# Kernel optimization log

Measured on AMD Instinct MI355X. Metric: run time of the kernel, lower is better.

Reference implementation:

```python
import jax, jax.numpy as jnp
import numpy as np
import math

B, T, D, H, V, L = 8, 512, 128, 512, 50257, 8
DT = 1.0
RAW_INIT = math.log(math.expm1(1.0))  # so softplus(raw) == 1.0


def setup_inputs() -> dict:
    key = jax.random.key(0)
    ks = jax.random.split(key, 8)
    x = jax.random.randint(ks[0], (B, T), 0, V)
    E = jax.random.normal(ks[1], (V, D), jnp.float32) * 0.02
    P = jax.random.normal(ks[2], (T, D), jnp.float32) * 0.01
    W0 = jax.random.normal(ks[3], (2 * D, H), jnp.float32) * 0.02
    W1 = jax.random.normal(ks[4], (H, H), jnp.float32) * 0.02
    W2 = jax.random.normal(ks[5], (H, H), jnp.float32) * 0.02
    W3 = jax.random.normal(ks[6], (H, 1), jnp.float32) * 0.002
    return {
        'x': x, 'E': E, 'P': P,
        'W0': W0, 'b0': jnp.zeros((H,), jnp.float32),
        'W1': W1, 'b1': jnp.zeros((H,), jnp.float32),
        'W2': W2, 'b2': jnp.zeros((H,), jnp.float32),
        'W3': W3, 'b3': jnp.zeros((1,), jnp.float32),
        'raw_m_bias': jnp.asarray(RAW_INIT, jnp.float32),
        'raw_gamma': jnp.asarray(RAW_INIT, jnp.float32),
    }


def causal_cumulative_mean(h):
    t = h.shape[1]
    denom = jnp.arange(1, t + 1, dtype=h.dtype)[None, :, None]
    return jnp.cumsum(h, axis=1) / denom


def mlp_energy_sum(xi, h, W0, b0, W1, b1, W2, b2, W3, b3):
    z = jnp.concatenate([xi, h], axis=-1)  # (B,T,2D)
    z = jax.nn.gelu(z @ W0 + b0, approximate=False)
    z = jax.nn.gelu(z @ W1 + b1, approximate=False)
    z = jax.nn.gelu(z @ W2 + b2, approximate=False)
    return jnp.sum(z @ W3 + b3)


def reference(x, E, P, W0, b0, W1, b1, W2, b2, W3, b3, raw_m_bias, raw_gamma):
    emb = E[x] + P[None, :T]  # (B,T,D)
    gamma = jax.nn.softplus(raw_gamma)
    m = jax.nn.softplus(raw_m_bias) + 0.001  # global mass
    h = emb
    v = jnp.zeros_like(h)
    for _ in range(L):
        # causal_force=True: xi built from detached h
        xi = causal_cumulative_mean(jax.lax.stop_gradient(h))
        grad_V = jax.grad(
            lambda hh: mlp_energy_sum(xi, hh, W0, b0, W1, b1, W2, b2, W3, b3)
        )(h)
        f = -grad_V
        v = (v + DT * f / m) / (1.0 + DT * gamma)
        h = h + DT * v
    logits = jnp.einsum('btd,vd->btv', h, E)  # (B,T,V)
    return logits
```

## Files before the change

### kernel.cpp

```cpp
#include <hip/hip_runtime.h>
#include <hip/hip_bf16.h>

typedef __attribute__((ext_vector_type(8))) short short8;
typedef __attribute__((ext_vector_type(4))) float f32x4;

#define DEV static __device__ __forceinline__

DEV void gelu_pair(float x, float& z, float& dz){
  float ax = fabsf(x)*0.70710678118654752f;
  float e  = __expf(-ax*ax);
  float t  = __fdividef(1.0f, 1.0f + 0.3275911f*ax);
  float poly = t*(0.254829592f + t*(-0.284496736f + t*(1.421413741f +
               t*(-1.453152027f + t*1.061405429f))));
  float erfv = 1.0f - poly*e;
  erfv = x < 0.0f ? -erfv : erfv;
  float cdf = 0.5f*(1.0f + erfv);
  z  = x*cdf;
  dz = cdf + x*0.39894228040143268f*e;
}
DEV float dgelu_f(float x){ float zz, dz; gelu_pair(x, zz, dz); return dz; }
DEV float softplus_f(float x){ return log1pf(expf(x)); }
DEV void store_f4_a4(float* p, f32x4 v){ __builtin_memcpy(p, &v, 16); }

DEV void gload_lds16(const __hip_bfloat16* g, __hip_bfloat16* l){
  __builtin_amdgcn_global_load_lds((const __attribute__((address_space(1))) void*)g,
                                   (__attribute__((address_space(3))) void*)l, 16, 0, 0);
}

DEV unsigned pack2bf(float a, float b){
  __hip_bfloat16 ba = __float2bfloat16(a), bb = __float2bfloat16(b);
  unsigned short ua, ub;
  __builtin_memcpy(&ua, &ba, 2); __builtin_memcpy(&ub, &bb, 2);
  return (unsigned)ua | ((unsigned)ub << 16);
}
DEV float unp_lo(unsigned u){ union{unsigned x; float f;} c; c.x = u << 16; return c.f; }
DEV float unp_hi(unsigned u){ union{unsigned x; float f;} c; c.x = u & 0xffff0000u; return c.f; }

__global__ __launch_bounds__(512) void embed_k(const int* __restrict__ x,
                        const float* __restrict__ E, const float* __restrict__ P,
                        float* __restrict__ h, float* __restrict__ S){
  int bid = blockIdx.x;
  int row = threadIdx.x >> 5;
  int q   = threadIdx.x & 31;
  int tok = bid*16 + row;
  int t   = tok & 511;
  int id  = x[tok];
  float4 e4 = ((const float4*)E)[(size_t)id*32 + q];
  float4 p4 = ((const float4*)P)[(size_t)t*32 + q];
  float4 val; val.x=e4.x+p4.x; val.y=e4.y+p4.y; val.z=e4.z+p4.z; val.w=e4.w+p4.w;
  ((float4*)h)[(size_t)tok*32 + q] = val;
  __shared__ float4 ps[16][32];
  ps[row][q] = val;
  __syncthreads();
  if (row==0){
    float4 s = ps[0][q];
    #pragma unroll
    for (int r=1;r<16;r++){
      float4 t4 = ps[r][q];
      s.x+=t4.x; s.y+=t4.y; s.z+=t4.z; s.w+=t4.w;
    }
    ((float4*)S)[(size_t)bid*32 + q] = s;
  }
}

__global__ void convw_k(const float* __restrict__ W0, const float* __restrict__ W1,
                        const float* __restrict__ W2,
                        __hip_bfloat16* __restrict__ W0T, __hip_bfloat16* __restrict__ W1T,
                        __hip_bfloat16* __restrict__ W2T, __hip_bfloat16* __restrict__ W2b,
                        __hip_bfloat16* __restrict__ W1b, __hip_bfloat16* __restrict__ W0h){
  int i = blockIdx.x*256 + threadIdx.x;
  if (i < 131072){
    int e=i&7, n=(i>>3)&511, kk=i>>12; int k=(kk>>2)*32+(kk&3)*8+e;
    W0T[i]=__float2bfloat16(W0[(size_t)k*512+n]);
  } else if (i < 393216){
    int j=i-131072; int e=j&7, n=(j>>3)&511, kk=j>>12; int k=(kk>>2)*32+(kk&3)*8+e;
    W1T[j]=__float2bfloat16(W1[(size_t)k*512+n]);
  } else if (i < 655360){
    int j=i-393216; int e=j&7, n=(j>>3)&511, kk=j>>12; int k=(kk>>2)*32+(kk&3)*8+e;
    W2T[j]=__float2bfloat16(W2[(size_t)k*512+n]);
  } else if (i < 917504){
    int j=i-655360; int e=j&7, n=(j>>3)&511, kk=j>>12; int k=(kk>>2)*32+(kk&3)*8+e;
    W2b[j]=__float2bfloat16(W2[(size_t)n*512+k]);
  } else if (i < 1179648){
    int j=i-917504; int e=j&7, n=(j>>3)&511, kk=j>>12; int k=(kk>>2)*32+(kk&3)*8+e;
    W1b[j]=__float2bfloat16(W1[(size_t)n*512+k]);
  } else if (i < 1245184){
    int j=i-1179648; int e=j&7, n=(j>>3)&127, kk=j>>10; int k=(kk>>2)*32+(kk&3)*8+e;
    W0h[j]=__float2bfloat16(W0[(size_t)(128+n)*512+k]);
  }
}
__global__ void conv_c4_k(const float* __restrict__ W, __hip_bfloat16* __restrict__ Wb, int n4){
  int i = blockIdx.x*256 + threadIdx.x;
  if (i < n4){
    float4 f = ((const float4*)W)[i];
    Wb[4*i+0]=__float2bfloat16(f.x);
    Wb[4*i+1]=__float2bfloat16(f.y);
    Wb[4*i+2]=__float2bfloat16(f.z);
    Wb[4*i+3]=__float2bfloat16(f.w);
  }
}

struct LayerP {
  const __hip_bfloat16 *W0T,*W1T,*W2T,*W2b,*W1b,*W0h;
  const float *b0,*b1,*b2,*W3;
  float *v, *h; __hip_bfloat16* hbf;
  const float* Sprev; float* Snext;
  const float *rawm,*rawg;
  int first, last;
};

template<int KSTEPS, int NW, int NF>
DEV void wpre(const __hip_bfloat16* __restrict__ Wt, int nbase, int r16, int g, int rot,
              short8 (&bb)[6][NF]){
  const __hip_bfloat16* wp = Wt + ((size_t)g*NW + nbase + r16)*8;
  #pragma unroll
  for (int d=0; d<5; d++){
    if (d < KSTEPS){
      int dd = (d + rot) & (KSTEPS-1);
      #pragma unroll
      for (int f=0; f<NF; f++)
        bb[d][f] = *(const short8*)&wp[((size_t)dd*4*NW + (size_t)f*16)*8];
    }
  }
}

template<int KSTEPS, int NW, int NF>
DEV void gphase(const __hip_bfloat16* __restrict__ Wt,
                const __hip_bfloat16* __restrict__ zin,
                int nbase, int r16, int g, int rot, f32x4 (&acc)[NF],
                short8 (&bb)[6][NF]){
  #pragma unroll
  for (int f=0;f<NF;f++) acc[f] = (f32x4){0.f,0.f,0.f,0.f};
  const __hip_bfloat16* wp = Wt + ((size_t)g*NW + nbase + r16)*8;
  #pragma unroll
  for (int s=0; s<KSTEPS; s++){
    if (s+5 < KSTEPS){
      int ss5 = (s + 5 + rot) & (KSTEPS-1);
      const __hip_bfloat16* wn = wp + (size_t)ss5*4*NW*8;
      #pragma unroll
      for (int f=0; f<NF; f++)
        bb[(s+5)%6][f] = *(const short8*)&wn[(size_t)f*128];
    }
    int ss = (s + rot) & (KSTEPS-1);
    short8 a = *(const short8*)&zin[(ss*4+g)*128 + r16*8];
    #pragma unroll
    for (int f=0; f<NF; f++)
      acc[f] = __builtin_amdgcn_mfma_f32_16x16x32_bf16(a, bb[s%6][f], acc[f],0,0,0);
  }
}

__global__ __launch_bounds__(1024,4) void layer_k(LayerP p){
  __shared__ __align__(16) __hip_bfloat16 sZ[2][8192];
  __shared__ float4 psum[16][32];
  __shared__ float4 psumC[16][32];
  const int tid = threadIdx.x;
  const int w = tid >> 6, lane = tid & 63;
  const int r16 = lane & 15, g = lane >> 4;
  const int rb = blockIdx.x;
  const int nb = w*32;
  const int rot = (rb >> 3) & 15;

  short8 bb[6][2];

  wpre<8,512,2>(p.W0T, nb, r16, g, rot, bb);
  float vr[4] = {0.f,0.f,0.f,0.f}, hr[4] = {0.f,0.f,0.f,0.f};
  float im = 0.f, fac = 0.f;
  if (w < 8){
    const int col = w*16 + r16;
    #pragma unroll
    for (int j=0;j<4;j++){
      size_t o = ((size_t)rb*16 + g*4 + j)*128 + col;
      hr[j] = p.h[o];
      vr[j] = p.first ? 0.f : p.v[o];
    }
    im  = 1.0f/(softplus_f(p.rawm[0]) + 0.001f);
    fac = 1.0f/(1.0f + softplus_f(p.rawg[0]));
  }

  if (tid < 512){
    const int row = tid >> 5;
    const int lane32 = tid & 31;
    const int b = rb >> 5, c = rb & 31;
    const float4* S4 = (const float4*)(p.Sprev + (size_t)b*32*128) + lane32;
    float4 part = {0.f,0.f,0.f,0.f};
    if (row < c){
      float4 t = S4[(size_t)row*32];
      part.x+=t.x; part.y+=t.y; part.z+=t.z; part.w+=t.w;
    }
    if (row+16 < c){
      float4 t = S4[(size_t)(row+16)*32];
      part.x+=t.x; part.y+=t.y; part.z+=t.z; part.w+=t.w;
    }
    float4 myrow = ((const float4*)(p.h + (size_t)rb*16*128))[(size_t)row*32 + lane32];
    psum[row][lane32]  = myrow;
    psumC[row][lane32] = part;
    __syncthreads();
    float4 pfx = {0.f,0.f,0.f,0.f};
    #pragma unroll
    for (int r=0;r<16;r++){
      float4 t = psumC[r][lane32];
      pfx.x+=t.x; pfx.y+=t.y; pfx.z+=t.z; pfx.w+=t.w;
    }
    #pragma unroll
    for (int rr=0; rr<15; rr++){
      float4 t = psum[rr][lane32];
      float sel = rr < row ? 1.0f : 0.0f;
      pfx.x += sel*t.x; pfx.y += sel*t.y; pfx.z += sel*t.z; pfx.w += sel*t.w;
    }
    pfx.x+=myrow.x; pfx.y+=myrow.y; pfx.z+=myrow.z; pfx.w+=myrow.w;
    float inv = 1.0f/(float)(c*16 + row + 1);
    const int d0 = lane32*4;
    union { ushort4 v; __hip_bfloat16 e[4]; } ux, uh;
    ux.e[0]=__float2bfloat16(pfx.x*inv); ux.e[1]=__float2bfloat16(pfx.y*inv);
    ux.e[2]=__float2bfloat16(pfx.z*inv); ux.e[3]=__float2bfloat16(pfx.w*inv);
    uh.e[0]=__float2bfloat16(myrow.x); uh.e[1]=__float2bfloat16(myrow.y);
    uh.e[2]=__float2bfloat16(myrow.z); uh.e[3]=__float2bfloat16(myrow.w);
    *(ushort4*)&sZ[0][(d0>>3)*128      + row*8 + (d0&7)] = ux.v;
    *(ushort4*)&sZ[0][(16+(d0>>3))*128 + row*8 + (d0&7)] = uh.v;
  } else {
    __syncthreads();
  }
  __syncthreads();

  f32x4 acc[2];
  unsigned g1p[2][2], g2p[2][2];

  gphase<8,512,2>(p.W0T, sZ[0], nb, r16, g, rot, acc, bb);
  wpre<16,512,2>(p.W1T, nb, r16, g, rot, bb);
  #pragma unroll
  for (int f=0; f<2; f++){
    int n = nb + f*16 + r16;
    float bias = p.b0[n];
    #pragma unroll
    for (int jp=0; jp<2; jp++){
      float z0, dz0, z1v, dz1;
      gelu_pair(acc[f][2*jp]   + bias, z0,  dz0);
      gelu_pair(acc[f][2*jp+1] + bias, z1v, dz1);
      g1p[f][jp] = pack2bf(dz0, dz1);
      sZ[1][(n>>3)*128 + (g*4+2*jp)*8   + (n&7)] = __float2bfloat16(z0);
      sZ[1][(n>>3)*128 + (g*4+2*jp+1)*8 + (n&7)] = __float2bfloat16(z1v);
    }
  }
  __syncthreads();

  gphase<16,512,2>(p.W1T, sZ[1], nb, r16, g, rot, acc, bb);
  wpre<16,512,2>(p.W2T, nb, r16, g, rot, bb);
  #pragma unroll
  for (int f=0; f<2; f++){
    int n = nb + f*16 + r16;
    float bias = p.b1[n];
    #pragma unroll
    for (int jp=0; jp<2; jp++){
      float z0, dz0, z1v, dz1;
      gelu_pair(acc[f][2*jp]   + bias, z0,  dz0);
      gelu_pair(acc[f][2*jp+1] + bias, z1v, dz1);
      g2p[f][jp] = pack2bf(dz0, dz1);
      sZ[0][(n>>3)*128 + (g*4+2*jp)*8   + (n&7)] = __float2bfloat16(z0);
      sZ[0][(n>>3)*128 + (g*4+2*jp+1)*8 + (n&7)] = __float2bfloat16(z1v);
    }
  }
  __syncthreads();

  gphase<16,512,2>(p.W2T, sZ[0], nb, r16, g, rot, acc, bb);
  wpre<16,512,2>(p.W2b, nb, r16, g, rot, bb);
  #pragma unroll
  for (int f=0; f<2; f++){
    int n = nb + f*16 + r16;
    float bias = p.b2[n];
    float w3 = p.W3[n];
    #pragma unroll
    for (int j=0;j<4;j++){
      float xx = acc[f][j] + bias;
      sZ[1][(n>>3)*128 + (g*4+j)*8 + (n&7)] = __float2bfloat16(w3*dgelu_f(xx));
    }
  }
  __syncthreads();

  gphase<16,512,2>(p.W2b, sZ[1], nb, r16, g, rot, acc, bb);
  wpre<16,512,2>(p.W1b, nb, r16, g, rot, bb);
  #pragma unroll
  for (int f=0; f<2; f++){
    int n = nb + f*16 + r16;
    #pragma unroll
    for (int jp=0; jp<2; jp++){
      float gv0 = unp_lo(g2p[f][jp]), gv1 = unp_hi(g2p[f][jp]);
      sZ[0][(n>>3)*128 + (g*4+2*jp)*8   + (n&7)] = __float2bfloat16(acc[f][2*jp]*gv0);
      sZ[0][(n>>3)*128 + (g*4+2*jp+1)*8 + (n&7)] = __float2bfloat16(acc[f][2*jp+1]*gv1);
    }
  }
  __syncthreads();

  gphase<16,512,2>(p.W1b, sZ[0], nb, r16, g, rot, acc, bb);
  short8 bbF[6][1];
  if (w < 8) wpre<16,128,1>(p.W0h, w*16, r16, g, rot, bbF);
  #pragma unroll
  for (int f=0; f<2; f++){
    int n = nb + f*16 + r16;
    #pragma unroll
    for (int jp=0; jp<2; jp++){
      float gv0 = unp_lo(g1p[f][jp]), gv1 = unp_hi(g1p[f][jp]);
      sZ[1][(n>>3)*128 + (g*4+2*jp)*8   + (n&7)] = __float2bfloat16(acc[f][2*jp]*gv0);
      sZ[1][(n>>3)*128 + (g*4+2*jp+1)*8 + (n&7)] = __float2bfloat16(acc[f][2*jp+1]*gv1);
    }
  }
  __syncthreads();

  if (w < 8){
    f32x4 accF[1];
    gphase<16,128,1>(p.W0h, sZ[1], w*16, r16, g, rot, accF, bbF);
    int col = w*16 + r16;
    float hs = 0.f;
    #pragma unroll
    for (int j=0;j<4;j++){
      int row = g*4 + j;
      size_t o = ((size_t)rb*16 + row)*128 + col;
      float nv = (vr[j] - accF[0][j]*im)*fac;
      float nh = hr[j] + nv;
      if (!p.last){ p.v[o] = nv; p.h[o] = nh; }
      else        { p.hbf[o] = __float2bfloat16(nh); }
      hs += nh;
    }
    if (!p.last){
      hs += __shfl_xor(hs, 16);
      hs += __shfl_xor(hs, 32);
      if (g==0) p.Snext[(size_t)rb*128 + col] = hs;
    }
  }
}

__global__ __launch_bounds__(256,4) void logits_k(const __hip_bfloat16* __restrict__ A,
                                                  const __hip_bfloat16* __restrict__ Bt,
                                                  float* __restrict__ out){
  constexpr int V = 50257;
  __shared__ __align__(16) __hip_bfloat16 sA[128*64];
  __shared__ __align__(16) __hip_bfloat16 sB[128*64];
  const int tid = threadIdx.x, lane = tid & 63, wave = tid >> 6;
  const int wg = ((blockIdx.x & 7) * 1572) + (blockIdx.x >> 3);
  const int mt = wg & 31, nt = wg >> 5;
  const int m0 = mt*128, n0 = nt*128;
  const int wm = (wave>>1)*64, wn = (wave&1)*64;
  const int r16 = lane & 15, g = lane >> 4;
  const int srow = tid >> 3;
  const int scol = ((tid & 7) ^ (srow & 7)) * 8;
  const int sx = (r16 & 7) * 8;
  f32x4 zero = {0.f,0.f,0.f,0.f};
  f32x4 acc[4][4];
  #pragma unroll
  for (int i=0;i<4;i++){ acc[i][0]=zero; acc[i][1]=zero; acc[i][2]=zero; acc[i][3]=zero; }

  auto stageA = [&](int ks){
    #pragma unroll
    for (int i=0;i<4;i++)
      gload_lds16(A + (size_t)(m0 + i*32 + srow)*128 + ks*64 + scol,
                  &sA[i*2048 + wave*512]);
  };
  auto stageB = [&](int ks){
    #pragma unroll
    for (int i=0;i<4;i++){
      int r = n0 + i*32 + srow; if (r > V-1) r = V-1;
      gload_lds16(Bt + (size_t)r*128 + ks*64 + scol,
                  &sB[i*2048 + wave*512]);
    }
  };
  stageA(0); stageB(0);
  __syncthreads();
  #pragma unroll
  for (int ks=0; ks<2; ks++){
    #pragma unroll
    for (int kk=0; kk<2; kk++){
      const int ko = kk*32 + g*8;
      short8 a[4], b[4];
      #pragma unroll
      for (int ti=0; ti<4; ti++) a[ti] = *(const short8*)&sA[(wm + ti*16 + r16)*64 + (ko ^ sx)];
      #pragma unroll
      for (int tj=0; tj<4; tj++) b[tj] = *(const short8*)&sB[(wn + tj*16 + r16)*64 + (ko ^ sx)];
      #pragma unroll
      for (int tb=0; tb<4; tb++)
        #pragma unroll
        for (int ta=0; ta<4; ta++)
          acc[tb][ta] = __builtin_amdgcn_mfma_f32_16x16x32_bf16(b[tb],a[ta],acc[tb][ta],0,0,0);
    }
    if (ks==0){
      __syncthreads();
      stageA(1); stageB(1);
      __syncthreads();
    }
  }
  #pragma unroll
  for (int tb=0; tb<4; tb++){
    #pragma unroll
    for (int ta=0; ta<4; ta++){
      int row = m0 + wm + ta*16 + r16;
      int n   = n0 + wn + tb*16 + g*4;
      f32x4 c = acc[tb][ta];
      float* po = out + (size_t)row*V + n;
      if (n + 3 < V){
        store_f4_a4(po, c);
      } else {
        #pragma unroll
        for (int j=0;j<4;j++) if (n+j < V) po[j] = c[j];
      }
    }
  }
}

extern "C" void kernel_launch(void* const* d_in, const int* in_sizes, int n_in,
                              void* d_out, int out_size, void* d_ws, size_t ws_size,
                              hipStream_t stream){
  const int*   x    = (const int*)  d_in[0];
  const float* E    = (const float*)d_in[1];
  const float* P    = (const float*)d_in[2];
  const float* W0   = (const float*)d_in[3];
  const float* b0   = (const float*)d_in[4];
  const float* W1   = (const float*)d_in[5];
  const float* b1   = (const float*)d_in[6];
  const float* W2   = (const float*)d_in[7];
  const float* b2   = (const float*)d_in[8];
  const float* W3   = (const float*)d_in[9];
  const float* rawm = (const float*)d_in[11];
  const float* rawg = (const float*)d_in[12];

  constexpr int B=8, T=512, D=128, H=512, V=50257, L=8;
  const int M = B*T;

  char* w = (char*)d_ws;
  auto alloc = [&](size_t bytes)->char*{ char* r = w; w += (bytes + 255) & ~(size_t)255; return r; };
  float* h            = (float*)alloc((size_t)M*D*4);
  float* v            = (float*)alloc((size_t)M*D*4);
  __hip_bfloat16* hbf = (__hip_bfloat16*)alloc((size_t)M*D*2);
  float* S0           = (float*)alloc((size_t)B*32*128*4);
  float* S1           = (float*)alloc((size_t)B*32*128*4);
  __hip_bfloat16* W0T = (__hip_bfloat16*)alloc((size_t)131072*2);
  __hip_bfloat16* W1T = (__hip_bfloat16*)alloc((size_t)262144*2);
  __hip_bfloat16* W2T = (__hip_bfloat16*)alloc((size_t)262144*2);
  __hip_bfloat16* W2b = (__hip_bfloat16*)alloc((size_t)262144*2);
  __hip_bfloat16* W1b = (__hip_bfloat16*)alloc((size_t)262144*2);
  __hip_bfloat16* W0h = (__hip_bfloat16*)alloc((size_t)65536*2);
  __hip_bfloat16* Ebf = (__hip_bfloat16*)alloc((size_t)V*D*2);

  convw_k  <<<4864, 256, 0, stream>>>(W0, W1, W2, W0T, W1T, W2T, W2b, W1b, W0h);
  conv_c4_k<<<(V*D/4+255)/256, 256, 0, stream>>>(E, Ebf, V*D/4);
  embed_k<<<M/16, 512, 0, stream>>>(x, E, P, h, S0);

  LayerP lp{};
  lp.W0T=W0T; lp.W1T=W1T; lp.W2T=W2T; lp.W2b=W2b; lp.W1b=W1b; lp.W0h=W0h;
  lp.b0=b0; lp.b1=b1; lp.b2=b2; lp.W3=W3;
  lp.v=v; lp.h=h; lp.hbf=hbf; lp.rawm=rawm; lp.rawg=rawg;

  for (int l=0; l<L; l++){
    lp.Sprev = (l&1) ? S1 : S0;
    lp.Snext = (l&1) ? S0 : S1;
    lp.first = (l==0) ? 1 : 0;
    lp.last  = (l==L-1) ? 1 : 0;
    layer_k<<<M/16, 1024, 0, stream>>>(lp);
  }
  logits_k<<<12576, 256, 0, stream>>>(hbf, Ebf, (float*)d_out);
}
```

Before: 562.9 us.

## Switch the layer MLP forward and backward GEMMs from bf16 to scaled fp8 MFMA

```diff
diff --git a/kernel.cpp b/kernel.cpp
--- a/kernel.cpp
+++ b/kernel.cpp
@@ -3,6 +3,7 @@
 
 typedef __attribute__((ext_vector_type(8))) short short8;
 typedef __attribute__((ext_vector_type(4))) float f32x4;
+typedef unsigned char u8;
 
 #define DEV static __device__ __forceinline__
 
@@ -27,6 +28,16 @@
                                    (__attribute__((address_space(3))) void*)l, 16, 0, 0);
 }
 
+DEV u8 f2fp8(float f){
+  int r = __builtin_amdgcn_cvt_pk_fp8_f32(f, f, 0, false);
+  return (u8)(r & 0xff);
+}
+DEV unsigned pk4_fp8(float a, float b, float c, float d){
+  int r = __builtin_amdgcn_cvt_pk_fp8_f32(a, b, 0, false);
+  r = __builtin_amdgcn_cvt_pk_fp8_f32(c, d, r, true);
+  return (unsigned)r;
+}
+
 DEV unsigned pack2bf(float a, float b){
   __hip_bfloat16 ba = __float2bfloat16(a), bb = __float2bfloat16(b);
   unsigned short ua, ub;
@@ -35,6 +46,20 @@
 }
 DEV float unp_lo(unsigned u){ union{unsigned x; float f;} c; c.x = u << 16; return c.f; }
 DEV float unp_hi(unsigned u){ union{unsigned x; float f;} c; c.x = u & 0xffff0000u; return c.f; }
+
+#define SW    32.0f
+#define SZC   32.0f
+#define SZ1   256.0f
+#define SZ2   1024.0f
+#define SG3   256.0f
+#define INV1  (1.0f/1024.0f)
+#define INV2  (1.0f/8192.0f)
+#define INV3  (1.0f/32768.0f)
+#define INV4  (1.0f/8192.0f)
+#define EN4   0.125f
+#define INV5  (1.0f/32768.0f)
+#define EN5   0.125f
+#define INV6  (1.0f/131072.0f)
 
 __global__ __launch_bounds__(512) void embed_k(const int* __restrict__ x,
                         const float* __restrict__ E, const float* __restrict__ P,
@@ -65,28 +90,28 @@
 
 __global__ void convw_k(const float* __restrict__ W0, const float* __restrict__ W1,
                         const float* __restrict__ W2,
-                        __hip_bfloat16* __restrict__ W0T, __hip_bfloat16* __restrict__ W1T,
-                        __hip_bfloat16* __restrict__ W2T, __hip_bfloat16* __restrict__ W2b,
-                        __hip_bfloat16* __restrict__ W1b, __hip_bfloat16* __restrict__ W0h){
+                        u8* __restrict__ W0T, u8* __restrict__ W1T,
+                        u8* __restrict__ W2T, u8* __restrict__ W2b,
+                        u8* __restrict__ W1b, u8* __restrict__ W0h){
   int i = blockIdx.x*256 + threadIdx.x;
   if (i < 131072){
     int e=i&7, n=(i>>3)&511, kk=i>>12; int k=(kk>>2)*32+(kk&3)*8+e;
-    W0T[i]=__float2bfloat16(W0[(size_t)k*512+n]);
+    W0T[i]=f2fp8(SW*W0[(size_t)k*512+n]);
   } else if (i < 393216){
     int j=i-131072; int e=j&7, n=(j>>3)&511, kk=j>>12; int k=(kk>>2)*32+(kk&3)*8+e;
-    W1T[j]=__float2bfloat16(W1[(size_t)k*512+n]);
+    W1T[j]=f2fp8(SW*W1[(size_t)k*512+n]);
   } else if (i < 655360){
     int j=i-393216; int e=j&7, n=(j>>3)&511, kk=j>>12; int k=(kk>>2)*32+(kk&3)*8+e;
-    W2T[j]=__float2bfloat16(W2[(size_t)k*512+n]);
+    W2T[j]=f2fp8(SW*W2[(size_t)k*512+n]);
   } else if (i < 917504){
     int j=i-655360; int e=j&7, n=(j>>3)&511, kk=j>>12; int k=(kk>>2)*32+(kk&3)*8+e;
-    W2b[j]=__float2bfloat16(W2[(size_t)n*512+k]);
+    W2b[j]=f2fp8(SW*W2[(size_t)n*512+k]);
   } else if (i < 1179648){
     int j=i-917504; int e=j&7, n=(j>>3)&511, kk=j>>12; int k=(kk>>2)*32+(kk&3)*8+e;
-    W1b[j]=__float2bfloat16(W1[(size_t)n*512+k]);
+    W1b[j]=f2fp8(SW*W1[(size_t)n*512+k]);
   } else if (i < 1245184){
     int j=i-1179648; int e=j&7, n=(j>>3)&127, kk=j>>10; int k=(kk>>2)*32+(kk&3)*8+e;
-    W0h[j]=__float2bfloat16(W0[(size_t)(128+n)*512+k]);
+    W0h[j]=f2fp8(SW*W0[(size_t)(128+n)*512+k]);
   }
 }
 __global__ void conv_c4_k(const float* __restrict__ W, __hip_bfloat16* __restrict__ Wb, int n4){
@@ -101,7 +126,7 @@
 }
 
 struct LayerP {
-  const __hip_bfloat16 *W0T,*W1T,*W2T,*W2b,*W1b,*W0h;
+  const u8 *W0T,*W1T,*W2T,*W2b,*W1b,*W0h;
   const float *b0,*b1,*b2,*W3;
   float *v, *h; __hip_bfloat16* hbf;
   const float* Sprev; float* Snext;
@@ -110,47 +135,47 @@
 };
 
 template<int KSTEPS, int NW, int NF>
-DEV void wpre(const __hip_bfloat16* __restrict__ Wt, int nbase, int r16, int g, int rot,
-              short8 (&bb)[6][NF]){
-  const __hip_bfloat16* wp = Wt + ((size_t)g*NW + nbase + r16)*8;
+DEV void wpre(const u8* __restrict__ Wt, int nbase, int r16, int g, int rot,
+              long (&bb)[6][NF]){
+  const u8* wp = Wt + ((size_t)g*NW + nbase + r16)*8;
   #pragma unroll
   for (int d=0; d<5; d++){
     if (d < KSTEPS){
       int dd = (d + rot) & (KSTEPS-1);
       #pragma unroll
       for (int f=0; f<NF; f++)
-        bb[d][f] = *(const short8*)&wp[((size_t)dd*4*NW + (size_t)f*16)*8];
+        bb[d][f] = *(const long*)&wp[((size_t)dd*4*NW + (size_t)f*16)*8];
     }
   }
 }
 
 template<int KSTEPS, int NW, int NF>
-DEV void gphase(const __hip_bfloat16* __restrict__ Wt,
-                const __hip_bfloat16* __restrict__ zin,
+DEV void gphase(const u8* __restrict__ Wt,
+                const u8* __restrict__ zin,
                 int nbase, int r16, int g, int rot, f32x4 (&acc)[NF],
-                short8 (&bb)[6][NF]){
+                long (&bb)[6][NF]){
   #pragma unroll
   for (int f=0;f<NF;f++) acc[f] = (f32x4){0.f,0.f,0.f,0.f};
-  const __hip_bfloat16* wp = Wt + ((size_t)g*NW + nbase + r16)*8;
+  const u8* wp = Wt + ((size_t)g*NW + nbase + r16)*8;
   #pragma unroll
   for (int s=0; s<KSTEPS; s++){
     if (s+5 < KSTEPS){
       int ss5 = (s + 5 + rot) & (KSTEPS-1);
-      const __hip_bfloat16* wn = wp + (size_t)ss5*4*NW*8;
+      const u8* wn = wp + (size_t)ss5*4*NW*8;
       #pragma unroll
       for (int f=0; f<NF; f++)
-        bb[(s+5)%6][f] = *(const short8*)&wn[(size_t)f*128];
+        bb[(s+5)%6][f] = *(const long*)&wn[(size_t)f*128];
     }
     int ss = (s + rot) & (KSTEPS-1);
-    short8 a = *(const short8*)&zin[(ss*4+g)*128 + r16*8];
+    long a = *(const long*)&zin[(ss*4+g)*128 + r16*8];
     #pragma unroll
     for (int f=0; f<NF; f++)
-      acc[f] = __builtin_amdgcn_mfma_f32_16x16x32_bf16(a, bb[s%6][f], acc[f],0,0,0);
+      acc[f] = __builtin_amdgcn_mfma_f32_16x16x32_fp8_fp8(a, bb[s%6][f], acc[f],0,0,0);
   }
 }
 
 __global__ __launch_bounds__(1024,4) void layer_k(LayerP p){
-  __shared__ __align__(16) __hip_bfloat16 sZ[2][8192];
+  __shared__ __align__(16) u8 sZ[2][8192];
   __shared__ float4 psum[16][32];
   __shared__ float4 psumC[16][32];
   const int tid = threadIdx.x;
@@ -160,7 +185,7 @@
   const int nb = w*32;
   const int rot = (rb >> 3) & 15;
 
-  short8 bb[6][2];
+  long bb[6][2];
 
   wpre<8,512,2>(p.W0T, nb, r16, g, rot, bb);
   float vr[4] = {0.f,0.f,0.f,0.f}, hr[4] = {0.f,0.f,0.f,0.f};
@@ -173,7 +198,7 @@
       hr[j] = p.h[o];
       vr[j] = p.first ? 0.f : p.v[o];
     }
-    im  = 1.0f/(softplus_f(p.rawm[0]) + 0.001f);
+    im  = INV6/(softplus_f(p.rawm[0]) + 0.001f);
     fac = 1.0f/(1.0f + softplus_f(p.rawg[0]));
   }
 
@@ -208,15 +233,12 @@
       pfx.x += sel*t.x; pfx.y += sel*t.y; pfx.z += sel*t.z; pfx.w += sel*t.w;
     }
     pfx.x+=myrow.x; pfx.y+=myrow.y; pfx.z+=myrow.z; pfx.w+=myrow.w;
-    float inv = 1.0f/(float)(c*16 + row + 1);
+    float inv32 = SZC/(float)(c*16 + row + 1);
     const int d0 = lane32*4;
-    union { ushort4 v; __hip_bfloat16 e[4]; } ux, uh;
-    ux.e[0]=__float2bfloat16(pfx.x*inv); ux.e[1]=__float2bfloat16(pfx.y*inv);
-    ux.e[2]=__float2bfloat16(pfx.z*inv); ux.e[3]=__float2bfloat16(pfx.w*inv);
-    uh.e[0]=__float2bfloat16(myrow.x); uh.e[1]=__float2bfloat16(myrow.y);
-    uh.e[2]=__float2bfloat16(myrow.z); uh.e[3]=__float2bfloat16(myrow.w);
-    *(ushort4*)&sZ[0][(d0>>3)*128      + row*8 + (d0&7)] = ux.v;
-    *(ushort4*)&sZ[0][(16+(d0>>3))*128 + row*8 + (d0&7)] = uh.v;
+    unsigned ux = pk4_fp8(pfx.x*inv32, pfx.y*inv32, pfx.z*inv32, pfx.w*inv32);
+    unsigned uh = pk4_fp8(myrow.x*SZC, myrow.y*SZC, myrow.z*SZC, myrow.w*SZC);
+    *(unsigned*)&sZ[0][(d0>>3)*128      + row*8 + (d0&7)] = ux;
+    *(unsigned*)&sZ[0][(16+(d0>>3))*128 + row*8 + (d0&7)] = uh;
   } else {
     __syncthreads();
   }
@@ -234,11 +256,11 @@
     #pragma unroll
     for (int jp=0; jp<2; jp++){
       float z0, dz0, z1v, dz1;
-      gelu_pair(acc[f][2*jp]   + bias, z0,  dz0);
-      gelu_pair(acc[f][2*jp+1] + bias, z1v, dz1);
+      gelu_pair(acc[f][2*jp]*INV1   + bias, z0,  dz0);
+      gelu_pair(acc[f][2*jp+1]*INV1 + bias, z1v, dz1);
       g1p[f][jp] = pack2bf(dz0, dz1);
-      sZ[1][(n>>3)*128 + (g*4+2*jp)*8   + (n&7)] = __float2bfloat16(z0);
-      sZ[1][(n>>3)*128 + (g*4+2*jp+1)*8 + (n&7)] = __float2bfloat16(z1v);
+      sZ[1][(n>>3)*128 + (g*4+2*jp)*8   + (n&7)] = f2fp8(z0*SZ1);
+      sZ[1][(n>>3)*128 + (g*4+2*jp+1)*8 + (n&7)] = f2fp8(z1v*SZ1);
     }
   }
   __syncthreads();
@@ -252,11 +274,11 @@
     #pragma unroll
     for (int jp=0; jp<2; jp++){
       float z0, dz0, z1v, dz1;
-      gelu_pair(acc[f][2*jp]   + bias, z0,  dz0);
-      gelu_pair(acc[f][2*jp+1] + bias, z1v, dz1);
+      gelu_pair(acc[f][2*jp]*INV2   + bias, z0,  dz0);
+      gelu_pair(acc[f][2*jp+1]*INV2 + bias, z1v, dz1);
       g2p[f][jp] = pack2bf(dz0, dz1);
-      sZ[0][(n>>3)*128 + (g*4+2*jp)*8   + (n&7)] = __float2bfloat16(z0);
-      sZ[0][(n>>3)*128 + (g*4+2*jp+1)*8 + (n&7)] = __float2bfloat16(z1v);
+      sZ[0][(n>>3)*128 + (g*4+2*jp)*8   + (n&7)] = f2fp8(z0*SZ2);
+      sZ[0][(n>>3)*128 + (g*4+2*jp+1)*8 + (n&7)] = f2fp8(z1v*SZ2);
     }
   }
   __syncthreads();
@@ -267,11 +289,11 @@
   for (int f=0; f<2; f++){
     int n = nb + f*16 + r16;
     float bias = p.b2[n];
-    float w3 = p.W3[n];
+    float w3s = p.W3[n]*SG3;
     #pragma unroll
     for (int j=0;j<4;j++){
-      float xx = acc[f][j] + bias;
-      sZ[1][(n>>3)*128 + (g*4+j)*8 + (n&7)] = __float2bfloat16(w3*dgelu_f(xx));
+      float xx = acc[f][j]*INV3 + bias;
+      sZ[1][(n>>3)*128 + (g*4+j)*8 + (n&7)] = f2fp8(w3s*dgelu_f(xx));
     }
   }
   __syncthreads();
@@ -284,14 +306,14 @@
     #pragma unroll
     for (int jp=0; jp<2; jp++){
       float gv0 = unp_lo(g2p[f][jp]), gv1 = unp_hi(g2p[f][jp]);
-      sZ[0][(n>>3)*128 + (g*4+2*jp)*8   + (n&7)] = __float2bfloat16(acc[f][2*jp]*gv0);
-      sZ[0][(n>>3)*128 + (g*4+2*jp+1)*8 + (n&7)] = __float2bfloat16(acc[f][2*jp+1]*gv1);
+      sZ[0][(n>>3)*128 + (g*4+2*jp)*8   + (n&7)] = f2fp8(acc[f][2*jp]*gv0*EN4);
+      sZ[0][(n>>3)*128 + (g*4+2*jp+1)*8 + (n&7)] = f2fp8(acc[f][2*jp+1]*gv1*EN4);
     }
   }
   __syncthreads();
 
   gphase<16,512,2>(p.W1b, sZ[0], nb, r16, g, rot, acc, bb);
-  short8 bbF[6][1];
+  long bbF[6][1];
   if (w < 8) wpre<16,128,1>(p.W0h, w*16, r16, g, rot, bbF);
   #pragma unroll
   for (int f=0; f<2; f++){
@@ -299,8 +321,8 @@
     #pragma unroll
     for (int jp=0; jp<2; jp++){
       float gv0 = unp_lo(g1p[f][jp]), gv1 = unp_hi(g1p[f][jp]);
-      sZ[1][(n>>3)*128 + (g*4+2*jp)*8   + (n&7)] = __float2bfloat16(acc[f][2*jp]*gv0);
-      sZ[1][(n>>3)*128 + (g*4+2*jp+1)*8 + (n&7)] = __float2bfloat16(acc[f][2*jp+1]*gv1);
+      sZ[1][(n>>3)*128 + (g*4+2*jp)*8   + (n&7)] = f2fp8(acc[f][2*jp]*gv0*EN5);
+      sZ[1][(n>>3)*128 + (g*4+2*jp+1)*8 + (n&7)] = f2fp8(acc[f][2*jp+1]*gv1*EN5);
     }
   }
   __syncthreads();
@@ -430,12 +452,12 @@
   __hip_bfloat16* hbf = (__hip_bfloat16*)alloc((size_t)M*D*2);
   float* S0           = (float*)alloc((size_t)B*32*128*4);
   float* S1           = (float*)alloc((size_t)B*32*128*4);
-  __hip_bfloat16* W0T = (__hip_bfloat16*)alloc((size_t)131072*2);
-  __hip_bfloat16* W1T = (__hip_bfloat16*)alloc((size_t)262144*2);
-  __hip_bfloat16* W2T = (__hip_bfloat16*)alloc((size_t)262144*2);
-  __hip_bfloat16* W2b = (__hip_bfloat16*)alloc((size_t)262144*2);
-  __hip_bfloat16* W1b = (__hip_bfloat16*)alloc((size_t)262144*2);
-  __hip_bfloat16* W0h = (__hip_bfloat16*)alloc((size_t)65536*2);
+  u8* W0T             = (u8*)alloc((size_t)131072);
+  u8* W1T             = (u8*)alloc((size_t)262144);
+  u8* W2T             = (u8*)alloc((size_t)262144);
+  u8* W2b             = (u8*)alloc((size_t)262144);
+  u8* W1b             = (u8*)alloc((size_t)262144);
+  u8* W0h             = (u8*)alloc((size_t)65536);
   __hip_bfloat16* Ebf = (__hip_bfloat16*)alloc((size_t)V*D*2);
 
   convw_k  <<<4864, 256, 0, stream>>>(W0, W1, W2, W0T, W1T, W2T, W2b, W1b, W0h);
```

After: 540.7 us. 1.04x faster.
